# Kernel optimization log

Measured on AMD Instinct MI355X. Metric: run time of the kernel, lower is better.

The kernel has to match this reference:

```python
import jax, jax.numpy as jnp
import numpy as np

E, D_IN, D_OUT, A, R, T = 8, 1024, 1024, 4, 16, 8192


def setup_inputs() -> dict:
    key = jax.random.key(0)
    ks = jax.random.split(key, 6)
    x = jax.random.normal(ks[0], (T, D_IN), jnp.float32)
    weight = jax.random.normal(ks[1], (E, D_IN, D_OUT), jnp.float32) / np.float32(np.sqrt(D_IN))
    # he_uniform-like scale for lora_A; lora_B random (zeros in real init would hide the LoRA path)
    lora_A = jax.random.normal(ks[2], (A, E, D_IN, R), jnp.float32) * np.float32(np.sqrt(2.0 / D_IN))
    lora_B = jax.random.normal(ks[3], (A, E, R, D_OUT), jnp.float32) * np.float32(0.02)
    lora_scaling = jax.random.uniform(ks[4], (A,), jnp.float32, 0.5, 1.5)
    group_sizes = jnp.full((E,), T // E, dtype=jnp.int32)  # sums to T
    adapter_indices_sorted = jax.random.randint(ks[5], (T,), 0, A, dtype=jnp.int32)
    return {
        'x': x, 'weight': weight, 'lora_A': lora_A, 'lora_B': lora_B,
        'lora_scaling': lora_scaling, 'group_sizes': group_sizes,
        'adapter_indices_sorted': adapter_indices_sorted,
    }


def reference(x, weight, lora_A, lora_B, lora_scaling, group_sizes, adapter_indices_sorted):
    total_tokens, d_in = x.shape
    n_experts, _, d_out = weight.shape
    n_adapters, _, _, rank = lora_A.shape
    n_groups = n_adapters * n_experts

    # Base expert-grouped GEMM: x is already sorted by expert via group_sizes.
    base_out = jax.lax.ragged_dot(x, weight, group_sizes)  # [T, d_out]

    # Combined (adapter, expert) group id per token.
    expert_idx = jnp.repeat(jnp.arange(n_experts), group_sizes, total_repeat_length=total_tokens)
    flat_idx = adapter_indices_sorted * n_experts + expert_idx  # [T]

    # prepare_routing: stable sort tokens by combined group id.
    sort_idx = jnp.argsort(flat_idx, stable=True)
    x_sorted = x[sort_idx]
    combined_group_sizes = jnp.zeros((n_groups,), jnp.int32).at[flat_idx].add(1)
    unsort_idx = jnp.argsort(sort_idx)

    # Nested LoRA grouped GEMMs over flattened (adapter, expert) groups.
    lora_A_flat = lora_A.reshape(n_groups, d_in, rank)
    lora_B_flat = lora_B.reshape(n_groups, rank, d_out)
    intermediate = jax.lax.ragged_dot(x_sorted, lora_A_flat, combined_group_sizes)  # [T, rank]
    lora_out_sorted = jax.lax.ragged_dot(intermediate, lora_B_flat, combined_group_sizes)  # [T, d_out]

    lora_out = lora_out_sorted[unsort_idx] * lora_scaling[adapter_indices_sorted, None]
    return base_out + lora_out
```

## Files before the change

### kernel.cpp

```cpp
#include <hip/hip_runtime.h>
#include <hip/hip_bf16.h>
#include <stdint.h>


#define T_TOK 8192
#define DIN   1024
#define DOUT  1024
#define NE    8
#define NA    4
#define RK    16
#define KEXT  1088
#define NOCT  136

typedef __attribute__((ext_vector_type(8))) short short8;
typedef __attribute__((ext_vector_type(4))) float f32x4;

__device__ __forceinline__ ushort f2bf(float f) {
  union { float f; uint32_t i; } v; v.f = f;
  uint32_t x = v.i;
  return (ushort)((x + 0x7fffu + ((x >> 16) & 1u)) >> 16);
}

__device__ __forceinline__ void gload_lds16(const void* g, void* l) {
  __builtin_amdgcn_global_load_lds(
      (const __attribute__((address_space(1))) uint32_t*)g,
      (__attribute__((address_space(3))) uint32_t*)l,
      16, 0, 0);
}

__device__ __forceinline__ int expert_of_row(const int* __restrict__ gs, int row) {
  int cum = 0, e = 0;
#pragma unroll
  for (int i = 0; i < NE; ++i) { if (row >= cum) e = i; cum += gs[i]; }
  return e;
}

__global__ __launch_bounds__(256) void k_prepA(
    const float* __restrict__ lora_A, const float* __restrict__ lora_scaling,
    ushort* __restrict__ Aoct) {
  const int bid = blockIdx.x;
  const int tid = threadIdx.x;
  int u = bid * 4 + (tid >> 6);
  int e = u >> 7, ko = u & 127;
  int c = tid & 63;
  int a = c >> 4, r = c & 15;
  float s = lora_scaling[a];
  ushort o8[8];
#pragma unroll
  for (int j = 0; j < 8; ++j) {
    float v = lora_A[((size_t)(a * NE + e) * DIN + ko * 8 + j) * RK + r];
    o8[j] = f2bf(s * v);
  }
  *(uint4*)(Aoct + ((size_t)((e * 128 + ko) * 64 + c)) * 8) = *(const uint4*)o8;
}

__global__ __launch_bounds__(256) void k_main(
    const float* __restrict__ x, ushort* __restrict__ xp,
    const ushort* __restrict__ Aoct,
    const float* __restrict__ weight, const float* __restrict__ lora_B,
    ushort* __restrict__ Boct,
    const int* __restrict__ gs, const int* __restrict__ adapter_idx) {
  __shared__ ushort As2[4 * 16 * 64];
  __shared__ ushort Bs2[4 * 8 * 64 * 8];

  const int bid = blockIdx.x;
  const int tid = threadIdx.x;

  if (bid < 512) {
    const int lane = tid & 63;
    const int wave = tid >> 6;
    const int rows0 = bid * 16;
    const int e = expert_of_row(gs, rows0);
    const ushort* aoct = Aoct + (size_t)e * 128 * 64 * 8;

    const int row = tid >> 4;
    const int seg = tid & 15;
    const int r7 = row & 7;
    const int t4 = seg >> 2;
    const int c0 = (seg & 3) * 2;

    f32x4 acc = (f32x4){0.f, 0.f, 0.f, 0.f};

    for (int it = 0; it < 4; ++it) {
#pragma unroll
      for (int i = 0; i < 8; ++i) {
        int t = i >> 1;
        int o = wave * 2 + (i & 1);
        const ushort* src = aoct + ((size_t)((it * 4 + t) * 8 + o) * 64 + lane) * 8;
        gload_lds16(src, &Bs2[((t * 8 + o) * 64) * 8]);
      }

      const float* srcx = x + (size_t)(rows0 + row) * DIN + it * 256 + seg * 16;
      float4 q0 = ((const float4*)srcx)[0];
      float4 q1 = ((const float4*)srcx)[1];
      float4 q2 = ((const float4*)srcx)[2];
      float4 q3 = ((const float4*)srcx)[3];
      ushort o16[16];
      o16[0]  = f2bf(q0.x); o16[1]  = f2bf(q0.y); o16[2]  = f2bf(q0.z); o16[3]  = f2bf(q0.w);
      o16[4]  = f2bf(q1.x); o16[5]  = f2bf(q1.y); o16[6]  = f2bf(q1.z); o16[7]  = f2bf(q1.w);
      o16[8]  = f2bf(q2.x); o16[9]  = f2bf(q2.y); o16[10] = f2bf(q2.z); o16[11] = f2bf(q2.w);
      o16[12] = f2bf(q3.x); o16[13] = f2bf(q3.y); o16[14] = f2bf(q3.z); o16[15] = f2bf(q3.w);

      ushort* dstg = xp + (size_t)(rows0 + row) * KEXT + it * 256 + seg * 16;
      *(uint4*)(dstg)     = ((const uint4*)o16)[0];
      *(uint4*)(dstg + 8) = ((const uint4*)o16)[1];

      *(uint4*)&As2[(t4 * 16 + row) * 64 + ((c0 ^ r7) * 8)]       = ((const uint4*)o16)[0];
      *(uint4*)&As2[(t4 * 16 + row) * 64 + (((c0 + 1) ^ r7) * 8)] = ((const uint4*)o16)[1];

      __syncthreads();

      int m = lane & 15;
#pragma unroll
      for (int t = 0; t < 4; ++t) {
#pragma unroll
        for (int h = 0; h < 2; ++h) {
          int kblk = h * 4 + (lane >> 4);
          short8 af = *(const short8*)&As2[(t * 16 + m) * 64 + (kblk ^ (m & 7)) * 8];
          short8 bfv = *(const short8*)&Bs2[((t * 8 + kblk) * 64 + wave * 16 + m) * 8];
          acc = __builtin_amdgcn_mfma_f32_16x16x32_bf16(af, bfv, acc, 0, 0, 0);
        }
      }
      __syncthreads();
    }

#pragma unroll
    for (int i = 0; i < 4; ++i) {
      int grow = rows0 + (lane >> 4) * 4 + i;
      int a_row = adapter_idx[grow];
      float val = (a_row == wave) ? acc[i] : 0.f;
      xp[(size_t)grow * KEXT + DIN + wave * 16 + (lane & 15)] = f2bf(val);
    }
  } else {
    int e, ko;
    const float* srcbase = nullptr;
    if (bid < 1536) {
      int u = bid - 512;
      e = u >> 7; ko = u & 127;
      srcbase = weight + (size_t)e * DIN * DOUT + (size_t)(ko * 8) * DOUT;
    } else {
      int u = bid - 1536;
      e = u >> 3; int o = u & 7; ko = 128 + o;
    }
    int n4 = tid * 4;
    float v[8][4];
    if (bid < 1536) {
#pragma unroll
      for (int j = 0; j < 8; ++j) {
        float4 q = *(const float4*)(srcbase + (size_t)j * DOUT + n4);
        v[j][0] = q.x; v[j][1] = q.y; v[j][2] = q.z; v[j][3] = q.w;
      }
    } else {
      int o = ko - 128;
#pragma unroll
      for (int j = 0; j < 8; ++j) {
        int kv = o * 8 + j;
        int a = kv >> 4, r = kv & 15;
        float4 q = *(const float4*)(lora_B + (size_t)((a * NE + e) * RK + r) * DOUT + n4);
        v[j][0] = q.x; v[j][1] = q.y; v[j][2] = q.z; v[j][3] = q.w;
      }
    }
    ushort* dst = Boct + ((size_t)(e * NOCT + ko) * DOUT + n4) * 8;
#pragma unroll
    for (int i = 0; i < 4; ++i) {
      ushort o8[8];
#pragma unroll
      for (int j = 0; j < 8; ++j) o8[j] = f2bf(v[j][i]);
      *(uint4*)(dst + i * 8) = *(const uint4*)o8;
    }
  }
}

__global__ __launch_bounds__(256) void k_gemm(
    const ushort* __restrict__ xp, const ushort* __restrict__ Boct,
    const int* __restrict__ gs, float* __restrict__ out) {
  __shared__ ushort As[2][128 * 64];
  __shared__ ushort Bs[2][8 * 128 * 8];

  const int tid = threadIdx.x;
  const int lane = tid & 63;
  const int wave = tid >> 6;
  const int wm = wave >> 1, wn = wave & 1;

  const int bid = blockIdx.x;
  const int swz = (bid & 7) * 64 + (bid >> 3);
  const int row0 = (swz >> 3) * 128;
  const int n0 = (swz & 7) * 128;
  const int e = expert_of_row(gs, row0);
  const ushort* boct = Boct + (size_t)e * NOCT * DOUT * 8;

  f32x4 acc[4][4];
#pragma unroll
  for (int mi = 0; mi < 4; ++mi)
#pragma unroll
    for (int ni = 0; ni < 4; ++ni) acc[mi][ni] = (f32x4){0.f, 0.f, 0.f, 0.f};

  const int r8 = lane >> 3;
  const int c8s = (lane & 7) ^ r8;

#define STAGE_TILE(hb, kt)                                                     \
  do {                                                                         \
    _Pragma("unroll")                                                          \
    for (int rd = 0; rd < 4; ++rd) {                                           \
      int r_ = wave * 32 + rd * 8 + r8;                                        \
      const ushort* src_ = xp + (size_t)(row0 + r_) * KEXT + (kt) * 64 + c8s * 8; \
      gload_lds16(src_, &As[hb][(wave * 32 + rd * 8) * 64]);                   \
    }                                                                          \
    _Pragma("unroll")                                                          \
    for (int rd = 0; rd < 4; ++rd) {                                           \
      int u_ = wave * 4 + rd;                                                  \
      int o_ = u_ >> 1, hf_ = u_ & 1;                                          \
      const ushort* src_ =                                                     \
          boct + ((size_t)((kt) * 8 + o_) * DOUT + n0 + hf_ * 64 + lane) * 8;  \
      gload_lds16(src_, &Bs[hb][(o_ * 128 + hf_ * 64) * 8]);                   \
    }                                                                          \
  } while (0)

#define COMPUTE_TILE(hb)                                                       \
  do {                                                                         \
    _Pragma("unroll")                                                          \
    for (int h = 0; h < 2; ++h) {                                              \
      int kblk = h * 4 + (lane >> 4);                                          \
      short8 af[4], bfv[4];                                                    \
      _Pragma("unroll")                                                        \
      for (int mi = 0; mi < 4; ++mi) {                                         \
        int m_ = wm * 64 + mi * 16 + (lane & 15);                              \
        af[mi] = *(const short8*)&As[hb][m_ * 64 + (kblk ^ (m_ & 7)) * 8];     \
      }                                                                        \
      _Pragma("unroll")                                                        \
      for (int ni = 0; ni < 4; ++ni) {                                         \
        int n_ = wn * 64 + ni * 16 + (lane & 15);                              \
        bfv[ni] = *(const short8*)&Bs[hb][(kblk * 128 + n_) * 8];              \
      }                                                                        \
      _Pragma("unroll")                                                        \
      for (int mi = 0; mi < 4; ++mi)                                           \
        _Pragma("unroll")                                                      \
        for (int ni = 0; ni < 4; ++ni)                                         \
          acc[mi][ni] = __builtin_amdgcn_mfma_f32_16x16x32_bf16(               \
              af[mi], bfv[ni], acc[mi][ni], 0, 0, 0);                          \
    }                                                                          \
  } while (0)

  for (int kp = 0; kp < 8; ++kp) {
    STAGE_TILE(0, kp * 2);
    STAGE_TILE(1, kp * 2 + 1);
    __syncthreads();
    COMPUTE_TILE(0);
    COMPUTE_TILE(1);
    __syncthreads();
  }
  STAGE_TILE(0, 16);
  __syncthreads();
  COMPUTE_TILE(0);

#undef STAGE_TILE
#undef COMPUTE_TILE

#pragma unroll
  for (int mi = 0; mi < 4; ++mi) {
#pragma unroll
    for (int ni = 0; ni < 4; ++ni) {
      int col = n0 + wn * 64 + ni * 16 + (lane & 15);
#pragma unroll
      for (int i = 0; i < 4; ++i) {
        int r = row0 + wm * 64 + mi * 16 + (lane >> 4) * 4 + i;
        out[(size_t)r * DOUT + col] = acc[mi][ni][i];
      }
    }
  }
}

extern "C" void kernel_launch(void* const* d_in, const int* in_sizes, int n_in,
                              void* d_out, int out_size, void* d_ws, size_t ws_size,
                              hipStream_t stream) {
  const float* x            = (const float*)d_in[0];
  const float* weight       = (const float*)d_in[1];
  const float* lora_A       = (const float*)d_in[2];
  const float* lora_B       = (const float*)d_in[3];
  const float* lora_scaling = (const float*)d_in[4];
  const int*   group_sizes  = (const int*)d_in[5];
  const int*   adapter_idx  = (const int*)d_in[6];
  float* out = (float*)d_out;

  const size_t sz_xp = (size_t)T_TOK * KEXT * 2;
  ushort* xp   = (ushort*)d_ws;
  ushort* boct = (ushort*)((char*)d_ws + sz_xp);
  ushort* aoct = (ushort*)((char*)d_ws + 2 * sz_xp);

  k_prepA<<<256, 256, 0, stream>>>(lora_A, lora_scaling, aoct);
  k_main<<<1600, 256, 0, stream>>>(x, xp, aoct, weight, lora_B, boct,
                                   group_sizes, adapter_idx);
  k_gemm<<<512, 256, 0, stream>>>(xp, boct, group_sizes, out);
}
```

Baseline: 152.7 us.

## Fuse LoRA-A projection into main GEMM instead of separate pre-pass

The LoRA-A intermediate (x times scaled A for all adapters) is now computed inside the main GEMM k-loop by reusing the already-staged x fragments with extra MFMAs against A read directly from global memory. After the loop, the masked intermediate is written to LDS and multiplied by the LoRA-B tile as a final k-step. This removes the separate LDS-staged A GEMM in the prep kernel and the extended-K column in the x buffer, which makes the prep kernel a plain convert. In exchange, each GEMM block recomputes the A projection redundantly across its 8 column tiles, adds 8 MFMAs per k-step and uncached-per-lane global loads inside the inner loop.

```diff
diff --git a/kernel.cpp b/kernel.cpp
--- a/kernel.cpp
+++ b/kernel.cpp
@@ -9,7 +9,6 @@
 #define NE    8
 #define NA    4
 #define RK    16
-#define KEXT  1088
 #define NOCT  136
 
 typedef __attribute__((ext_vector_type(8))) short short8;
@@ -56,95 +55,34 @@
 
 __global__ __launch_bounds__(256) void k_main(
     const float* __restrict__ x, ushort* __restrict__ xp,
-    const ushort* __restrict__ Aoct,
     const float* __restrict__ weight, const float* __restrict__ lora_B,
-    ushort* __restrict__ Boct,
-    const int* __restrict__ gs, const int* __restrict__ adapter_idx) {
-  __shared__ ushort As2[4 * 16 * 64];
-  __shared__ ushort Bs2[4 * 8 * 64 * 8];
-
+    ushort* __restrict__ Boct) {
   const int bid = blockIdx.x;
   const int tid = threadIdx.x;
 
-  if (bid < 512) {
-    const int lane = tid & 63;
-    const int wave = tid >> 6;
-    const int rows0 = bid * 16;
-    const int e = expert_of_row(gs, rows0);
-    const ushort* aoct = Aoct + (size_t)e * 128 * 64 * 8;
-
-    const int row = tid >> 4;
-    const int seg = tid & 15;
-    const int r7 = row & 7;
-    const int t4 = seg >> 2;
-    const int c0 = (seg & 3) * 2;
-
-    f32x4 acc = (f32x4){0.f, 0.f, 0.f, 0.f};
-
-    for (int it = 0; it < 4; ++it) {
-#pragma unroll
-      for (int i = 0; i < 8; ++i) {
-        int t = i >> 1;
-        int o = wave * 2 + (i & 1);
-        const ushort* src = aoct + ((size_t)((it * 4 + t) * 8 + o) * 64 + lane) * 8;
-        gload_lds16(src, &Bs2[((t * 8 + o) * 64) * 8]);
-      }
-
-      const float* srcx = x + (size_t)(rows0 + row) * DIN + it * 256 + seg * 16;
-      float4 q0 = ((const float4*)srcx)[0];
-      float4 q1 = ((const float4*)srcx)[1];
-      float4 q2 = ((const float4*)srcx)[2];
-      float4 q3 = ((const float4*)srcx)[3];
-      ushort o16[16];
-      o16[0]  = f2bf(q0.x); o16[1]  = f2bf(q0.y); o16[2]  = f2bf(q0.z); o16[3]  = f2bf(q0.w);
-      o16[4]  = f2bf(q1.x); o16[5]  = f2bf(q1.y); o16[6]  = f2bf(q1.z); o16[7]  = f2bf(q1.w);
-      o16[8]  = f2bf(q2.x); o16[9]  = f2bf(q2.y); o16[10] = f2bf(q2.z); o16[11] = f2bf(q2.w);
-      o16[12] = f2bf(q3.x); o16[13] = f2bf(q3.y); o16[14] = f2bf(q3.z); o16[15] = f2bf(q3.w);
-
-      ushort* dstg = xp + (size_t)(rows0 + row) * KEXT + it * 256 + seg * 16;
-      *(uint4*)(dstg)     = ((const uint4*)o16)[0];
-      *(uint4*)(dstg + 8) = ((const uint4*)o16)[1];
-
-      *(uint4*)&As2[(t4 * 16 + row) * 64 + ((c0 ^ r7) * 8)]       = ((const uint4*)o16)[0];
-      *(uint4*)&As2[(t4 * 16 + row) * 64 + (((c0 + 1) ^ r7) * 8)] = ((const uint4*)o16)[1];
-
-      __syncthreads();
-
-      int m = lane & 15;
-#pragma unroll
-      for (int t = 0; t < 4; ++t) {
-#pragma unroll
-        for (int h = 0; h < 2; ++h) {
-          int kblk = h * 4 + (lane >> 4);
-          short8 af = *(const short8*)&As2[(t * 16 + m) * 64 + (kblk ^ (m & 7)) * 8];
-          short8 bfv = *(const short8*)&Bs2[((t * 8 + kblk) * 64 + wave * 16 + m) * 8];
-          acc = __builtin_amdgcn_mfma_f32_16x16x32_bf16(af, bfv, acc, 0, 0, 0);
-        }
-      }
-      __syncthreads();
-    }
-
-#pragma unroll
-    for (int i = 0; i < 4; ++i) {
-      int grow = rows0 + (lane >> 4) * 4 + i;
-      int a_row = adapter_idx[grow];
-      float val = (a_row == wave) ? acc[i] : 0.f;
-      xp[(size_t)grow * KEXT + DIN + wave * 16 + (lane & 15)] = f2bf(val);
+  if (bid < 1024) {
+#pragma unroll
+    for (int i = 0; i < 8; ++i) {
+      int u = bid * 2048 + i * 256 + tid;
+      float4 v = ((const float4*)x)[u];
+      ushort4 b;
+      b.x = f2bf(v.x); b.y = f2bf(v.y); b.z = f2bf(v.z); b.w = f2bf(v.w);
+      ((ushort4*)xp)[u] = b;
     }
   } else {
     int e, ko;
     const float* srcbase = nullptr;
-    if (bid < 1536) {
-      int u = bid - 512;
+    if (bid < 2048) {
+      int u = bid - 1024;
       e = u >> 7; ko = u & 127;
       srcbase = weight + (size_t)e * DIN * DOUT + (size_t)(ko * 8) * DOUT;
     } else {
-      int u = bid - 1536;
+      int u = bid - 2048;
       e = u >> 3; int o = u & 7; ko = 128 + o;
     }
     int n4 = tid * 4;
     float v[8][4];
-    if (bid < 1536) {
+    if (bid < 2048) {
 #pragma unroll
       for (int j = 0; j < 8; ++j) {
         float4 q = *(const float4*)(srcbase + (size_t)j * DOUT + n4);
@@ -173,7 +111,9 @@
 
 __global__ __launch_bounds__(256) void k_gemm(
     const ushort* __restrict__ xp, const ushort* __restrict__ Boct,
-    const int* __restrict__ gs, float* __restrict__ out) {
+    const ushort* __restrict__ Aoct,
+    const int* __restrict__ gs, const int* __restrict__ adapter_idx,
+    float* __restrict__ out) {
   __shared__ ushort As[2][128 * 64];
   __shared__ ushort Bs[2][8 * 128 * 8];
 
@@ -188,12 +128,17 @@
   const int n0 = (swz & 7) * 128;
   const int e = expert_of_row(gs, row0);
   const ushort* boct = Boct + (size_t)e * NOCT * DOUT * 8;
+  const ushort* aocte = Aoct + (size_t)e * 128 * 64 * 8;
 
   f32x4 acc[4][4];
-#pragma unroll
-  for (int mi = 0; mi < 4; ++mi)
+  f32x4 vacc[4][2];
+#pragma unroll
+  for (int mi = 0; mi < 4; ++mi) {
 #pragma unroll
     for (int ni = 0; ni < 4; ++ni) acc[mi][ni] = (f32x4){0.f, 0.f, 0.f, 0.f};
+    vacc[mi][0] = (f32x4){0.f, 0.f, 0.f, 0.f};
+    vacc[mi][1] = (f32x4){0.f, 0.f, 0.f, 0.f};
+  }
 
   const int r8 = lane >> 3;
   const int c8s = (lane & 7) ^ r8;
@@ -203,7 +148,7 @@
     _Pragma("unroll")                                                          \
     for (int rd = 0; rd < 4; ++rd) {                                           \
       int r_ = wave * 32 + rd * 8 + r8;                                        \
-      const ushort* src_ = xp + (size_t)(row0 + r_) * KEXT + (kt) * 64 + c8s * 8; \
+      const ushort* src_ = xp + (size_t)(row0 + r_) * DIN + (kt) * 64 + c8s * 8; \
       gload_lds16(src_, &As[hb][(wave * 32 + rd * 8) * 64]);                   \
     }                                                                          \
     _Pragma("unroll")                                                          \
@@ -216,11 +161,16 @@
     }                                                                          \
   } while (0)
 
-#define COMPUTE_TILE(hb)                                                       \
+#define COMPUTE_TILE(hb, kt)                                                   \
   do {                                                                         \
     _Pragma("unroll")                                                          \
     for (int h = 0; h < 2; ++h) {                                              \
       int kblk = h * 4 + (lane >> 4);                                          \
+                  \
+      short8 av0 = *(const short8*)(aocte +                                    \
+          ((size_t)((kt) * 8 + kblk) * 64 + wn * 32 + (lane & 15)) * 8);       \
+      short8 av1 = *(const short8*)(aocte +                                    \
+          ((size_t)((kt) * 8 + kblk) * 64 + wn * 32 + 16 + (lane & 15)) * 8);  \
       short8 af[4], bfv[4];                                                    \
       _Pragma("unroll")                                                        \
       for (int mi = 0; mi < 4; ++mi) {                                         \
@@ -238,6 +188,13 @@
         for (int ni = 0; ni < 4; ++ni)                                         \
           acc[mi][ni] = __builtin_amdgcn_mfma_f32_16x16x32_bf16(               \
               af[mi], bfv[ni], acc[mi][ni], 0, 0, 0);                          \
+      _Pragma("unroll")                                                        \
+      for (int mi = 0; mi < 4; ++mi) {                                         \
+        vacc[mi][0] = __builtin_amdgcn_mfma_f32_16x16x32_bf16(                 \
+            af[mi], av0, vacc[mi][0], 0, 0, 0);                                \
+        vacc[mi][1] = __builtin_amdgcn_mfma_f32_16x16x32_bf16(                 \
+            af[mi], av1, vacc[mi][1], 0, 0, 0);                                \
+      }                                                                        \
     }                                                                          \
   } while (0)
 
@@ -245,16 +202,58 @@
     STAGE_TILE(0, kp * 2);
     STAGE_TILE(1, kp * 2 + 1);
     __syncthreads();
-    COMPUTE_TILE(0);
-    COMPUTE_TILE(1);
+    COMPUTE_TILE(0, kp * 2);
+    COMPUTE_TILE(1, kp * 2 + 1);
     __syncthreads();
   }
-  STAGE_TILE(0, 16);
-  __syncthreads();
-  COMPUTE_TILE(0);
 
 #undef STAGE_TILE
 #undef COMPUTE_TILE
+
+#pragma unroll
+  for (int rd = 0; rd < 4; ++rd) {
+    int u = wave * 4 + rd;
+    int o = u >> 1, hf = u & 1;
+    const ushort* src = boct + ((size_t)(128 + o) * DOUT + n0 + hf * 64 + lane) * 8;
+    gload_lds16(src, &Bs[0][(o * 128 + hf * 64) * 8]);
+  }
+#pragma unroll
+  for (int mi = 0; mi < 4; ++mi) {
+#pragma unroll
+    for (int i = 0; i < 4; ++i) {
+      int rl = wm * 64 + mi * 16 + (lane >> 4) * 4 + i;
+      int arow = adapter_idx[row0 + rl];
+#pragma unroll
+      for (int vi = 0; vi < 2; ++vi) {
+        int c = wn * 32 + vi * 16 + (lane & 15);
+        float val = (arow == (wn * 2 + vi)) ? vacc[mi][vi][i] : 0.f;
+        As[0][rl * 64 + (((c >> 3) ^ (rl & 7)) * 8) + (c & 7)] = f2bf(val);
+      }
+    }
+  }
+  __syncthreads();
+
+#pragma unroll
+  for (int h = 0; h < 2; ++h) {
+    int kblk = h * 4 + (lane >> 4);
+    short8 af[4], bfv[4];
+#pragma unroll
+    for (int mi = 0; mi < 4; ++mi) {
+      int m = wm * 64 + mi * 16 + (lane & 15);
+      af[mi] = *(const short8*)&As[0][m * 64 + (kblk ^ (m & 7)) * 8];
+    }
+#pragma unroll
+    for (int ni = 0; ni < 4; ++ni) {
+      int n = wn * 64 + ni * 16 + (lane & 15);
+      bfv[ni] = *(const short8*)&Bs[0][(kblk * 128 + n) * 8];
+    }
+#pragma unroll
+    for (int mi = 0; mi < 4; ++mi)
+#pragma unroll
+      for (int ni = 0; ni < 4; ++ni)
+        acc[mi][ni] = __builtin_amdgcn_mfma_f32_16x16x32_bf16(
+            af[mi], bfv[ni], acc[mi][ni], 0, 0, 0);
+  }
 
 #pragma unroll
   for (int mi = 0; mi < 4; ++mi) {
@@ -282,13 +281,13 @@
   const int*   adapter_idx  = (const int*)d_in[6];
   float* out = (float*)d_out;
 
-  const size_t sz_xp = (size_t)T_TOK * KEXT * 2;
+  const size_t sz_xp   = (size_t)T_TOK * DIN * 2;
+  const size_t sz_boct = (size_t)NE * NOCT * DOUT * 8 * 2;
   ushort* xp   = (ushort*)d_ws;
   ushort* boct = (ushort*)((char*)d_ws + sz_xp);
-  ushort* aoct = (ushort*)((char*)d_ws + 2 * sz_xp);
+  ushort* aoct = (ushort*)((char*)d_ws + sz_xp + sz_boct);
 
   k_prepA<<<256, 256, 0, stream>>>(lora_A, lora_scaling, aoct);
-  k_main<<<1600, 256, 0, stream>>>(x, xp, aoct, weight, lora_B, boct,
-                                   group_sizes, adapter_idx);
-  k_gemm<<<512, 256, 0, stream>>>(xp, boct, group_sizes, out);
-}
+  k_main<<<2112, 256, 0, stream>>>(x, xp, weight, lora_B, boct);
+  k_gemm<<<512, 256, 0, stream>>>(xp, boct, aoct, group_sizes, adapter_idx, out);
+}
```

Measured after the change: 175.9 us. 15.2% more time.

## Split-K LoRA-A projection across waves and move x bf16 conversion to separate blocks

Applied to the files above, without the earlier changes.

The LoRA-A projection blocks now split the K dimension across the four waves. Each wave computes all four adapters' rank outputs from registers and global loads, without LDS staging, and the partial sums are reduced through shared memory. The x-to-bf16 conversion and store into the extended activation buffer moves into 1024 separate blocks, so the grid grows to 2624. The row-block index is also swizzled across experts. The aim is to shorten the serial K loop and remove per-iteration barriers in the projection blocks, at the cost of reading x twice and more block launches.

```diff
diff --git a/kernel.cpp b/kernel.cpp
--- a/kernel.cpp
+++ b/kernel.cpp
@@ -60,91 +60,90 @@
     const float* __restrict__ weight, const float* __restrict__ lora_B,
     ushort* __restrict__ Boct,
     const int* __restrict__ gs, const int* __restrict__ adapter_idx) {
-  __shared__ ushort As2[4 * 16 * 64];
-  __shared__ ushort Bs2[4 * 8 * 64 * 8];
+  __shared__ float vred[4][16][65];
 
   const int bid = blockIdx.x;
   const int tid = threadIdx.x;
 
   if (bid < 512) {
+    const int vb = (bid & 7) * 64 + (bid >> 3);
     const int lane = tid & 63;
     const int wave = tid >> 6;
-    const int rows0 = bid * 16;
+    const int rows0 = vb * 16;
     const int e = expert_of_row(gs, rows0);
-    const ushort* aoct = Aoct + (size_t)e * 128 * 64 * 8;
-
-    const int row = tid >> 4;
-    const int seg = tid & 15;
-    const int r7 = row & 7;
-    const int t4 = seg >> 2;
-    const int c0 = (seg & 3) * 2;
-
-    f32x4 acc = (f32x4){0.f, 0.f, 0.f, 0.f};
-
-    for (int it = 0; it < 4; ++it) {
-#pragma unroll
-      for (int i = 0; i < 8; ++i) {
-        int t = i >> 1;
-        int o = wave * 2 + (i & 1);
-        const ushort* src = aoct + ((size_t)((it * 4 + t) * 8 + o) * 64 + lane) * 8;
-        gload_lds16(src, &Bs2[((t * 8 + o) * 64) * 8]);
-      }
-
-      const float* srcx = x + (size_t)(rows0 + row) * DIN + it * 256 + seg * 16;
-      float4 q0 = ((const float4*)srcx)[0];
-      float4 q1 = ((const float4*)srcx)[1];
-      float4 q2 = ((const float4*)srcx)[2];
-      float4 q3 = ((const float4*)srcx)[3];
-      ushort o16[16];
-      o16[0]  = f2bf(q0.x); o16[1]  = f2bf(q0.y); o16[2]  = f2bf(q0.z); o16[3]  = f2bf(q0.w);
-      o16[4]  = f2bf(q1.x); o16[5]  = f2bf(q1.y); o16[6]  = f2bf(q1.z); o16[7]  = f2bf(q1.w);
-      o16[8]  = f2bf(q2.x); o16[9]  = f2bf(q2.y); o16[10] = f2bf(q2.z); o16[11] = f2bf(q2.w);
-      o16[12] = f2bf(q3.x); o16[13] = f2bf(q3.y); o16[14] = f2bf(q3.z); o16[15] = f2bf(q3.w);
-
-      ushort* dstg = xp + (size_t)(rows0 + row) * KEXT + it * 256 + seg * 16;
-      *(uint4*)(dstg)     = ((const uint4*)o16)[0];
-      *(uint4*)(dstg + 8) = ((const uint4*)o16)[1];
-
-      *(uint4*)&As2[(t4 * 16 + row) * 64 + ((c0 ^ r7) * 8)]       = ((const uint4*)o16)[0];
-      *(uint4*)&As2[(t4 * 16 + row) * 64 + (((c0 + 1) ^ r7) * 8)] = ((const uint4*)o16)[1];
-
-      __syncthreads();
-
-      int m = lane & 15;
-#pragma unroll
-      for (int t = 0; t < 4; ++t) {
-#pragma unroll
-        for (int h = 0; h < 2; ++h) {
-          int kblk = h * 4 + (lane >> 4);
-          short8 af = *(const short8*)&As2[(t * 16 + m) * 64 + (kblk ^ (m & 7)) * 8];
-          short8 bfv = *(const short8*)&Bs2[((t * 8 + kblk) * 64 + wave * 16 + m) * 8];
-          acc = __builtin_amdgcn_mfma_f32_16x16x32_bf16(af, bfv, acc, 0, 0, 0);
-        }
-      }
-      __syncthreads();
-    }
-
-#pragma unroll
-    for (int i = 0; i < 4; ++i) {
-      int grow = rows0 + (lane >> 4) * 4 + i;
-      int a_row = adapter_idx[grow];
-      float val = (a_row == wave) ? acc[i] : 0.f;
-      xp[(size_t)grow * KEXT + DIN + wave * 16 + (lane & 15)] = f2bf(val);
+    const int m = lane & 15;
+    const int kg = lane >> 4;
+    const ushort* aocte = Aoct + (size_t)e * 128 * 64 * 8;
+    const float* xr = x + (size_t)(rows0 + m) * DIN;
+
+    f32x4 acc[4];
+#pragma unroll
+    for (int a = 0; a < 4; ++a) acc[a] = (f32x4){0.f, 0.f, 0.f, 0.f};
+
+    for (int kti = 0; kti < 8; ++kti) {
+      const int kb = wave * 256 + kti * 32;
+      const int k0 = kb + kg * 8;
+      float4 a0 = *(const float4*)(xr + k0);
+      float4 a1 = *(const float4*)(xr + k0 + 4);
+      short8 af;
+      af[0] = (short)f2bf(a0.x); af[1] = (short)f2bf(a0.y);
+      af[2] = (short)f2bf(a0.z); af[3] = (short)f2bf(a0.w);
+      af[4] = (short)f2bf(a1.x); af[5] = (short)f2bf(a1.y);
+      af[6] = (short)f2bf(a1.z); af[7] = (short)f2bf(a1.w);
+      const ushort* ab = aocte + ((size_t)(((kb >> 3) + kg) * 64) + m) * 8;
+#pragma unroll
+      for (int a = 0; a < 4; ++a) {
+        short8 bf = *(const short8*)(ab + (size_t)(a * 16) * 8);
+        acc[a] = __builtin_amdgcn_mfma_f32_16x16x32_bf16(af, bf, acc[a], 0, 0, 0);
+      }
+    }
+
+#pragma unroll
+    for (int a = 0; a < 4; ++a)
+#pragma unroll
+      for (int i = 0; i < 4; ++i)
+        vred[wave][kg * 4 + i][a * 16 + m] = acc[a][i];
+    __syncthreads();
+
+    int row = tid >> 4;
+    int c0 = (tid & 15) * 4;
+    float s0 = vred[0][row][c0]     + vred[1][row][c0]     + vred[2][row][c0]     + vred[3][row][c0];
+    float s1 = vred[0][row][c0 + 1] + vred[1][row][c0 + 1] + vred[2][row][c0 + 1] + vred[3][row][c0 + 1];
+    float s2 = vred[0][row][c0 + 2] + vred[1][row][c0 + 2] + vred[2][row][c0 + 2] + vred[3][row][c0 + 2];
+    float s3 = vred[0][row][c0 + 3] + vred[1][row][c0 + 3] + vred[2][row][c0 + 3] + vred[3][row][c0 + 3];
+    int arow = adapter_idx[rows0 + row];
+    bool on = (arow == (c0 >> 4));
+    ushort4 b;
+    b.x = f2bf(on ? s0 : 0.f);
+    b.y = f2bf(on ? s1 : 0.f);
+    b.z = f2bf(on ? s2 : 0.f);
+    b.w = f2bf(on ? s3 : 0.f);
+    *(ushort4*)(xp + (size_t)(rows0 + row) * KEXT + DIN + c0) = b;
+  } else if (bid < 1536) {
+#pragma unroll
+    for (int i = 0; i < 8; ++i) {
+      int u = (bid - 512) * 2048 + i * 256 + tid;
+      int row = u >> 8;
+      int c4 = u & 255;
+      float4 v = *(const float4*)(x + (size_t)row * DIN + c4 * 4);
+      ushort4 b;
+      b.x = f2bf(v.x); b.y = f2bf(v.y); b.z = f2bf(v.z); b.w = f2bf(v.w);
+      *(ushort4*)(xp + (size_t)row * KEXT + c4 * 4) = b;
     }
   } else {
     int e, ko;
     const float* srcbase = nullptr;
-    if (bid < 1536) {
-      int u = bid - 512;
+    if (bid < 2560) {
+      int u = bid - 1536;
       e = u >> 7; ko = u & 127;
       srcbase = weight + (size_t)e * DIN * DOUT + (size_t)(ko * 8) * DOUT;
     } else {
-      int u = bid - 1536;
+      int u = bid - 2560;
       e = u >> 3; int o = u & 7; ko = 128 + o;
     }
     int n4 = tid * 4;
     float v[8][4];
-    if (bid < 1536) {
+    if (bid < 2560) {
 #pragma unroll
       for (int j = 0; j < 8; ++j) {
         float4 q = *(const float4*)(srcbase + (size_t)j * DOUT + n4);
@@ -282,13 +281,14 @@
   const int*   adapter_idx  = (const int*)d_in[6];
   float* out = (float*)d_out;
 
-  const size_t sz_xp = (size_t)T_TOK * KEXT * 2;
+  const size_t sz_xp   = (size_t)T_TOK * KEXT * 2;
+  const size_t sz_boct = (size_t)NE * NOCT * DOUT * 8 * 2;
   ushort* xp   = (ushort*)d_ws;
   ushort* boct = (ushort*)((char*)d_ws + sz_xp);
-  ushort* aoct = (ushort*)((char*)d_ws + 2 * sz_xp);
+  ushort* aoct = (ushort*)((char*)d_ws + sz_xp + sz_boct);
 
   k_prepA<<<256, 256, 0, stream>>>(lora_A, lora_scaling, aoct);
-  k_main<<<1600, 256, 0, stream>>>(x, xp, aoct, weight, lora_B, boct,
+  k_main<<<2624, 256, 0, stream>>>(x, xp, aoct, weight, lora_B, boct,
                                    group_sizes, adapter_idx);
   k_gemm<<<512, 256, 0, stream>>>(xp, boct, group_sizes, out);
 }
```

New measurement: 154.3 us. No clear change (+1.1%).
